# Optimization experiments

Measured on AMD Instinct MI355X. Metric: run time of the kernel, lower is better.

The kernel has to match this reference:

```python
import jax, jax.numpy as jnp
import numpy as np

B, S, D = 4, 2048, 512
H, DK = 8, 64
FFN = 2048
LEFT, CHUNK, RIGHT = 512, 128, 128
EPS = 1e-5


def _emformer_mask():
    # True = disallowed. Each query attends to its own chunk, LEFT keys before
    # the chunk start, and RIGHT keys after the chunk end.
    idx = jnp.arange(S)
    cs = (idx // CHUNK) * CHUNK                      # chunk start per query
    j = idx[None, :]
    allowed = (j >= cs[:, None] - LEFT) & (j < cs[:, None] + CHUNK + RIGHT)
    return jnp.broadcast_to(~allowed, (B, 1, S, S))


def _ln(x, g, b):
    m = jnp.mean(x, axis=-1, keepdims=True)
    v = jnp.var(x, axis=-1, keepdims=True)
    return (x - m) * jax.lax.rsqrt(v + EPS) * g + b


def setup_inputs() -> dict:
    key = jax.random.key(0)
    ks = jax.random.split(key, 8)
    w = lambda k, shp: jax.random.normal(k, shp, dtype=jnp.float32) * 0.02
    return {
        "x": jax.random.normal(ks[0], (B, S, D), dtype=jnp.float32),
        "mask": _emformer_mask(),
        "ln_in_g": jnp.ones((D,), jnp.float32), "ln_in_b": jnp.zeros((D,), jnp.float32),
        "wq": w(ks[1], (D, D)), "bq": jnp.zeros((D,), jnp.float32),
        "wk": w(ks[2], (D, D)), "bk": jnp.zeros((D,), jnp.float32),
        "wv": w(ks[3], (D, D)), "bv": jnp.zeros((D,), jnp.float32),
        "ln1_g": jnp.ones((D,), jnp.float32), "ln1_b": jnp.zeros((D,), jnp.float32),
        "w1": w(ks[4], (D, FFN)), "b1": jnp.zeros((FFN,), jnp.float32),
        "w2": w(ks[5], (FFN, D)), "b2": jnp.zeros((D,), jnp.float32),
        "ln2_g": jnp.ones((D,), jnp.float32), "ln2_b": jnp.zeros((D,), jnp.float32),
    }


def reference(x, mask, ln_in_g, ln_in_b, wq, bq, wk, bk, wv, bv,
              ln1_g, ln1_b, w1, b1, w2, b2, ln2_g, ln2_b):
    h = _ln(x, ln_in_g, ln_in_b)                                  # [B,S,D]
    q = (h @ wq + bq).reshape(B, S, H, DK).transpose(0, 2, 1, 3)   # [B,H,S,DK]
    k = (h @ wk + bk).reshape(B, S, H, DK).transpose(0, 2, 1, 3)
    v = (h @ wv + bv).reshape(B, S, H, DK).transpose(0, 2, 1, 3)
    scores = jnp.einsum("bhqd,bhkd->bhqk", q, k) / np.sqrt(DK).astype(np.float32)
    scores = jnp.where(mask, -jnp.inf, scores)
    probs = jax.nn.softmax(scores, axis=-1)
    probs = jnp.where(mask, 0.0, probs)                           # masked_fill after softmax
    out = jnp.einsum("bhqk,bhkd->bhqd", probs, v)
    out = out.transpose(0, 2, 1, 3).reshape(B, S, D)
    attn_out = out + h                                            # residual uses post-LN input
    o = _ln(attn_out, ln1_g, ln1_b)
    o = (o @ w1 + b1) @ w2 + b2 + attn_out                        # NOTE: no activation in source
    return _ln(o, ln2_g, ln2_b)
```

## Files before the change

### kernel.cpp

```cpp
#include <hip/hip_runtime.h>
#include <stdint.h>

#define B_ 4
#define S_ 2048
#define D_ 512
#define H_ 8
#define FFN_ 2048
#define M_ (B_*S_)

typedef unsigned short u16;
typedef __attribute__((ext_vector_type(8))) __bf16 bf16x8;
typedef __attribute__((ext_vector_type(8))) u16 u16x8;
typedef __attribute__((ext_vector_type(4))) float f32x4;

__device__ __forceinline__ u16 f2bf(float f) {
  uint32_t u = __builtin_bit_cast(uint32_t, f);
  u += 0x7FFFu + ((u >> 16) & 1u);
  return (u16)(u >> 16);
}
__device__ __forceinline__ bf16x8 ldfrag(const u16* p) {
  return __builtin_bit_cast(bf16x8, *(const u16x8*)p);
}
__device__ __forceinline__ void gld16(const void* g, void* l) {
  __builtin_amdgcn_global_load_lds(
      (const __attribute__((address_space(1))) void*)g,
      (__attribute__((address_space(3))) void*)l, 16, 0, 0);
}

__global__ __launch_bounds__(256)
void wtrans(const float* __restrict__ W, int K, int N, u16* __restrict__ Wt) {
  __shared__ float t[32][33];
  int n0 = blockIdx.x * 32, k0 = blockIdx.y * 32;
  int x = threadIdx.x, y = threadIdx.y;
#pragma unroll
  for (int r = 0; r < 4; r++) t[y + 8*r][x] = W[(size_t)(k0 + y + 8*r) * N + n0 + x];
  __syncthreads();
#pragma unroll
  for (int r = 0; r < 4; r++) Wt[(size_t)(n0 + y + 8*r) * K + k0 + x] = f2bf(t[x][y + 8*r]);
}

__global__ void bcat(const float* __restrict__ bq, const float* __restrict__ bk,
                     const float* __restrict__ bv, float* __restrict__ o) {
  int i = blockIdx.x * 256 + threadIdx.x;
  o[i] = i < 512 ? bq[i] : (i < 1024 ? bk[i - 512] : bv[i - 1024]);
}

template <bool OUT32, bool OUT16>
__global__ __launch_bounds__(128)
void ln_k(const float* __restrict__ x, const float* __restrict__ g,
          const float* __restrict__ bta, float* __restrict__ y32, u16* __restrict__ y16) {
  int row = blockIdx.x;
  int t = threadIdx.x;
  const float* xr = x + (size_t)row * 512;
  f32x4 v = *(const f32x4*)(xr + t * 4);
  float s = v.x + v.y + v.z + v.w;
  float s2 = v.x*v.x + v.y*v.y + v.z*v.z + v.w*v.w;
#pragma unroll
  for (int m = 32; m; m >>= 1) { s += __shfl_xor(s, m); s2 += __shfl_xor(s2, m); }
  __shared__ float p[4];
  int wv = t >> 6;
  if ((t & 63) == 0) { p[wv] = s; p[2 + wv] = s2; }
  __syncthreads();
  s = p[0] + p[1]; s2 = p[2] + p[3];
  float mean = s * (1.f / 512.f);
  float var = s2 * (1.f / 512.f) - mean * mean;
  float rs = rsqrtf(var + 1e-5f);
#pragma unroll
  for (int j = 0; j < 4; j++) {
    float o = (v[j] - mean) * rs * g[t*4 + j] + bta[t*4 + j];
    if constexpr (OUT32) y32[(size_t)row * 512 + t*4 + j] = o;
    if constexpr (OUT16) y16[(size_t)row * 512 + t*4 + j] = f2bf(o);
  }
}

template <bool RESID, bool OUT32, bool OUT16>
__global__ __launch_bounds__(256)
void gemm_bt(const u16* __restrict__ A, const u16* __restrict__ Bt,
             const float* __restrict__ bias, int K, int N,
             const float* __restrict__ resid, float* __restrict__ C32,
             u16* __restrict__ C16) {
  __shared__ __align__(16) u16 As[128 * 32];
  __shared__ __align__(16) u16 Bs[128 * 32];
  const int tid = threadIdx.x;
  const int wave = tid >> 6, lane = tid & 63;
  const int l15 = lane & 15, quad = lane >> 4;
  const int wm = wave >> 1, wn = wave & 1;
  const int row0 = blockIdx.y * 128, col0 = blockIdx.x * 128;

  f32x4 acc[4][4];
#pragma unroll
  for (int i = 0; i < 4; i++)
#pragma unroll
    for (int j = 0; j < 4; j++) acc[i][j] = (f32x4){0.f, 0.f, 0.f, 0.f};

  const int lr = lane >> 2, lc = (lane & 3) * 8;
  const int ch0 = wave * 2, ch1 = wave * 2 + 1;
  const u16* aG0 = A + (size_t)(row0 + ch0 * 16 + lr) * K + lc;
  const u16* aG1 = A + (size_t)(row0 + ch1 * 16 + lr) * K + lc;
  const u16* bG0 = Bt + (size_t)(col0 + ch0 * 16 + lr) * K + lc;
  const u16* bG1 = Bt + (size_t)(col0 + ch1 * 16 + lr) * K + lc;
  u16* aL0 = As + ch0 * 512 + lane * 8;
  u16* aL1 = As + ch1 * 512 + lane * 8;
  u16* bL0 = Bs + ch0 * 512 + lane * 8;
  u16* bL1 = Bs + ch1 * 512 + lane * 8;

  for (int k0 = 0; k0 < K; k0 += 32) {
    __syncthreads();
    gld16(aG0 + k0, aL0);
    gld16(aG1 + k0, aL1);
    gld16(bG0 + k0, bL0);
    gld16(bG1 + k0, bL1);
    __syncthreads();
    bf16x8 af[4], bf[4];
#pragma unroll
    for (int mt = 0; mt < 4; mt++) af[mt] = ldfrag(As + (wm*64 + mt*16 + l15) * 32 + quad * 8);
#pragma unroll
    for (int nt = 0; nt < 4; nt++) bf[nt] = ldfrag(Bs + (wn*64 + nt*16 + l15) * 32 + quad * 8);
#pragma unroll
    for (int mt = 0; mt < 4; mt++)
#pragma unroll
      for (int nt = 0; nt < 4; nt++)
        acc[mt][nt] = __builtin_amdgcn_mfma_f32_16x16x32_bf16(af[mt], bf[nt], acc[mt][nt], 0, 0, 0);
  }
#pragma unroll
  for (int mt = 0; mt < 4; mt++)
#pragma unroll
    for (int nt = 0; nt < 4; nt++) {
      int n = col0 + wn * 64 + nt * 16 + l15;
      float bv = bias[n];
#pragma unroll
      for (int r = 0; r < 4; r++) {
        int m = row0 + wm * 64 + mt * 16 + quad * 4 + r;
        float val = acc[mt][nt][r] + bv;
        if constexpr (RESID) val += resid[(size_t)m * N + n];
        if constexpr (OUT32) C32[(size_t)m * N + n] = val;
        if constexpr (OUT16) C16[(size_t)m * N + n] = f2bf(val);
      }
    }
}

__global__ __launch_bounds__(256)
void vtrans(const u16* __restrict__ qkv, u16* __restrict__ vt) {
  __shared__ u16 t[64][65];
  int s0 = blockIdx.x * 64, h = blockIdx.y, b = blockIdx.z;
  int x = threadIdx.x, y = threadIdx.y;
  const u16* src = qkv + (size_t)(b * 2048 + s0) * 1536 + 1024 + h * 64;
#pragma unroll
  for (int r = 0; r < 16; r++) { int s = y + 4*r; t[s][x] = src[(size_t)s * 1536 + x]; }
  __syncthreads();
  u16* dst = vt + (size_t)((b * 8 + h) * 64) * 2048 + s0;
#pragma unroll
  for (int r = 0; r < 16; r++) { int d = y + 4*r; dst[(size_t)d * 2048 + x] = t[x][d]; }
}

#define PSTR 136
__global__ __launch_bounds__(256)
void attn_k(const u16* __restrict__ qkv, const u16* __restrict__ vt,
            const float* __restrict__ hres, float* __restrict__ attn) {
  __shared__ __align__(16) u16 smem[8192 + 8192 + 64 * PSTR];
  u16* Ks = smem;
  u16* Vts = smem + 8192;
  u16* Ps = smem + 16384;
  u16* Qs = Ps;

  const int c2 = blockIdx.x, hh = blockIdx.y, b = blockIdx.z;
  const int c = c2 >> 1;
  const int s0 = c2 * 64;
  const int tid = threadIdx.x, wave = tid >> 6, lane = tid & 63;
  const int l15 = lane & 15, quad = lane >> 4;
  const int t_lo = (c > 4) ? c - 4 : 0;
  const int t_hi = (c + 2 < 16) ? c + 2 : 16;

  {
    int d8 = (lane & 7) * 8;
#pragma unroll
    for (int q2 = 0; q2 < 2; q2++) {
      int r = wave * 16 + q2 * 8 + (lane >> 3);
      gld16(qkv + (size_t)(b * 2048 + s0 + r) * 1536 + hh * 64 + d8, Qs + r * 64 + d8);
    }
  }
  __syncthreads();
  bf16x8 qf[2];
#pragma unroll
  for (int f = 0; f < 2; f++)
    qf[f] = ldfrag(Qs + (wave * 16 + l15) * 64 + f * 32 + quad * 8);

  f32x4 accO[4];
#pragma unroll
  for (int i = 0; i < 4; i++) accO[i] = (f32x4){0.f, 0.f, 0.f, 0.f};
  float den[4] = {0.f, 0.f, 0.f, 0.f};

  for (int kt = t_lo; kt < t_hi; ++kt) {
    __syncthreads();
    {
      int d8 = (lane & 7) * 8;
#pragma unroll
      for (int q2 = 0; q2 < 4; q2++) {
        int r = wave * 32 + q2 * 8 + (lane >> 3);
        gld16(qkv + (size_t)(b * 2048 + kt * 128 + r) * 1536 + 512 + hh * 64 + d8,
              Ks + r * 64 + d8);
      }
      int sp = (lane & 15) * 8;
#pragma unroll
      for (int q2 = 0; q2 < 4; q2++) {
        int d = (wave * 4 + q2) * 4 + (lane >> 4);
        gld16(vt + (size_t)((b * 8 + hh) * 64 + d) * 2048 + kt * 128 + sp,
              Vts + d * 128 + sp);
      }
    }
    __syncthreads();

    float pv[8][4];
#pragma unroll
    for (int nt = 0; nt < 8; nt++) {
      f32x4 s4 = (f32x4){0.f, 0.f, 0.f, 0.f};
#pragma unroll
      for (int f = 0; f < 2; f++) {
        bf16x8 kf = ldfrag(Ks + (nt * 16 + l15) * 64 + f * 32 + quad * 8);
        s4 = __builtin_amdgcn_mfma_f32_16x16x32_bf16(qf[f], kf, s4, 0, 0, 0);
      }
#pragma unroll
      for (int r = 0; r < 4; r++) {
        float pp = exp2f(s4[r] * (1.4426950408889634f * 0.125f));
        pv[nt][r] = pp;
        den[r] += pp;
      }
    }
#pragma unroll
    for (int nt = 0; nt < 8; nt++)
#pragma unroll
      for (int r = 0; r < 4; r++)
        Ps[(wave * 16 + quad * 4 + r) * PSTR + nt * 16 + l15] = f2bf(pv[nt][r]);
#pragma unroll
    for (int ki = 0; ki < 4; ki++) {
      bf16x8 pf = ldfrag(Ps + (wave * 16 + l15) * PSTR + ki * 32 + quad * 8);
#pragma unroll
      for (int dt = 0; dt < 4; dt++) {
        bf16x8 vf = ldfrag(Vts + (dt * 16 + l15) * 128 + ki * 32 + quad * 8);
        accO[dt] = __builtin_amdgcn_mfma_f32_16x16x32_bf16(pf, vf, accO[dt], 0, 0, 0);
      }
    }
  }
#pragma unroll
  for (int r = 0; r < 4; r++) {
    float d = den[r];
    d += __shfl_xor(d, 1); d += __shfl_xor(d, 2);
    d += __shfl_xor(d, 4); d += __shfl_xor(d, 8);
    den[r] = d;
  }
#pragma unroll
  for (int dt = 0; dt < 4; dt++)
#pragma unroll
    for (int r = 0; r < 4; r++) {
      int m = s0 + wave * 16 + quad * 4 + r;
      size_t idx = (size_t)(b * 2048 + m) * 512 + hh * 64 + dt * 16 + l15;
      attn[idx] = accO[dt][r] / den[r] + hres[idx];
    }
}

extern "C" void kernel_launch(void* const* d_in, const int* in_sizes, int n_in,
                              void* d_out, int out_size, void* d_ws, size_t ws_size,
                              hipStream_t stream) {
  (void)in_sizes; (void)n_in; (void)out_size; (void)ws_size;
  const float* x       = (const float*)d_in[0];
  const float* ln_in_g = (const float*)d_in[2];
  const float* ln_in_b = (const float*)d_in[3];
  const float* wq = (const float*)d_in[4];
  const float* bq = (const float*)d_in[5];
  const float* wk = (const float*)d_in[6];
  const float* bk = (const float*)d_in[7];
  const float* wv = (const float*)d_in[8];
  const float* bv = (const float*)d_in[9];
  const float* ln1_g = (const float*)d_in[10];
  const float* ln1_b = (const float*)d_in[11];
  const float* w1 = (const float*)d_in[12];
  const float* b1 = (const float*)d_in[13];
  const float* w2 = (const float*)d_in[14];
  const float* b2 = (const float*)d_in[15];
  const float* ln2_g = (const float*)d_in[16];
  const float* ln2_b = (const float*)d_in[17];

  char* ws = (char*)d_ws;
  size_t off = 0;
  auto alloc = [&](size_t bytes) {
    void* p = ws + off;
    off = (off + bytes + 255) & ~(size_t)255;
    return p;
  };
  u16*   wqkvt = (u16*)  alloc((size_t)1536 * 512 * 2);
  float* bqkv  = (float*)alloc(1536 * 4);
  u16*   w1t   = (u16*)  alloc((size_t)2048 * 512 * 2);
  u16*   w2t   = (u16*)  alloc((size_t)512 * 2048 * 2);
  float* h32   = (float*)alloc((size_t)M_ * 512 * 4);
  u16*   h16   = (u16*)  alloc((size_t)M_ * 512 * 2);
  u16*   qkv16 = (u16*)  alloc((size_t)M_ * 1536 * 2);
  u16*   vtb   = (u16*)  alloc((size_t)B_ * H_ * 64 * 2048 * 2);
  float* attn32= (float*)alloc((size_t)M_ * 512 * 4);
  float* out2  = h32;
  u16*   o16   = h16;
  u16*   f16b  = qkv16;

  wtrans<<<dim3(16, 16), dim3(32, 8), 0, stream>>>(wq, 512, 512, wqkvt);
  wtrans<<<dim3(16, 16), dim3(32, 8), 0, stream>>>(wk, 512, 512, wqkvt + (size_t)512 * 512);
  wtrans<<<dim3(16, 16), dim3(32, 8), 0, stream>>>(wv, 512, 512, wqkvt + (size_t)1024 * 512);
  wtrans<<<dim3(64, 16), dim3(32, 8), 0, stream>>>(w1, 512, 2048, w1t);
  wtrans<<<dim3(16, 64), dim3(32, 8), 0, stream>>>(w2, 2048, 512, w2t);
  bcat<<<6, 256, 0, stream>>>(bq, bk, bv, bqkv);

  ln_k<true, true><<<M_, 128, 0, stream>>>(x, ln_in_g, ln_in_b, h32, h16);
  gemm_bt<false, false, true><<<dim3(12, 64), 256, 0, stream>>>(
      h16, wqkvt, bqkv, 512, 1536, nullptr, nullptr, qkv16);
  vtrans<<<dim3(32, 8, 4), dim3(64, 4), 0, stream>>>(qkv16, vtb);
  attn_k<<<dim3(32, 8, 4), 256, 0, stream>>>(qkv16, vtb, h32, attn32);
  ln_k<false, true><<<M_, 128, 0, stream>>>(attn32, ln1_g, ln1_b, nullptr, o16);
  gemm_bt<false, false, true><<<dim3(16, 64), 256, 0, stream>>>(
      o16, w1t, b1, 512, 2048, nullptr, nullptr, f16b);
  gemm_bt<true, true, false><<<dim3(4, 64), 256, 0, stream>>>(
      f16b, w2t, b2, 2048, 512, attn32, out2, nullptr);
  ln_k<true, false><<<M_, 128, 0, stream>>>(out2, ln2_g, ln2_b, (float*)d_out, nullptr);
}
```

Baseline: 334.8 us.

## Swizzle LDS layouts, widen attention block to full chunk, narrow FFN2 tiles

```diff
diff --git a/kernel.cpp b/kernel.cpp
--- a/kernel.cpp
+++ b/kernel.cpp
@@ -73,60 +73,67 @@
   }
 }
 
-template <bool RESID, bool OUT32, bool OUT16>
+template <int NTW, bool RESID, bool OUT32, bool OUT16>
 __global__ __launch_bounds__(256)
 void gemm_bt(const u16* __restrict__ A, const u16* __restrict__ Bt,
              const float* __restrict__ bias, int K, int N,
              const float* __restrict__ resid, float* __restrict__ C32,
              u16* __restrict__ C16) {
   __shared__ __align__(16) u16 As[128 * 32];
-  __shared__ __align__(16) u16 Bs[128 * 32];
+  __shared__ __align__(16) u16 Bs[NTW * 1024];
   const int tid = threadIdx.x;
   const int wave = tid >> 6, lane = tid & 63;
   const int l15 = lane & 15, quad = lane >> 4;
   const int wm = wave >> 1, wn = wave & 1;
-  const int row0 = blockIdx.y * 128, col0 = blockIdx.x * 128;
-
-  f32x4 acc[4][4];
+  const int row0 = blockIdx.y * 128, col0 = blockIdx.x * (NTW * 32);
+
+  f32x4 acc[4][NTW];
 #pragma unroll
   for (int i = 0; i < 4; i++)
 #pragma unroll
-    for (int j = 0; j < 4; j++) acc[i][j] = (f32x4){0.f, 0.f, 0.f, 0.f};
-
-  const int lr = lane >> 2, lc = (lane & 3) * 8;
-  const int ch0 = wave * 2, ch1 = wave * 2 + 1;
-  const u16* aG0 = A + (size_t)(row0 + ch0 * 16 + lr) * K + lc;
-  const u16* aG1 = A + (size_t)(row0 + ch1 * 16 + lr) * K + lc;
-  const u16* bG0 = Bt + (size_t)(col0 + ch0 * 16 + lr) * K + lc;
-  const u16* bG1 = Bt + (size_t)(col0 + ch1 * 16 + lr) * K + lc;
-  u16* aL0 = As + ch0 * 512 + lane * 8;
-  u16* aL1 = As + ch1 * 512 + lane * 8;
-  u16* bL0 = Bs + ch0 * 512 + lane * 8;
-  u16* bL1 = Bs + ch1 * 512 + lane * 8;
+    for (int j = 0; j < NTW; j++) acc[i][j] = (f32x4){0.f, 0.f, 0.f, 0.f};
+
+  const int lr = lane >> 2;
+  const int lc = ((lane & 3) ^ ((lane >> 3) & 3)) * 8;
+  const u16* aG0 = A + (size_t)(row0 + (wave * 2) * 16 + lr) * K + lc;
+  const u16* aG1 = A + (size_t)(row0 + (wave * 2 + 1) * 16 + lr) * K + lc;
+  u16* aL0 = As + (wave * 2) * 512 + lane * 8;
+  u16* aL1 = As + (wave * 2 + 1) * 512 + lane * 8;
+  const u16* bG[NTW / 2];
+  u16* bL[NTW / 2];
+#pragma unroll
+  for (int i = 0; i < NTW / 2; i++) {
+    int ch = wave * (NTW / 2) + i;
+    bG[i] = Bt + (size_t)(col0 + ch * 16 + lr) * K + lc;
+    bL[i] = Bs + ch * 512 + lane * 8;
+  }
+  const int rsw = (l15 >> 1) & 3;
 
   for (int k0 = 0; k0 < K; k0 += 32) {
     __syncthreads();
     gld16(aG0 + k0, aL0);
     gld16(aG1 + k0, aL1);
-    gld16(bG0 + k0, bL0);
-    gld16(bG1 + k0, bL1);
+#pragma unroll
+    for (int i = 0; i < NTW / 2; i++) gld16(bG[i] + k0, bL[i]);
     __syncthreads();
-    bf16x8 af[4], bf[4];
-#pragma unroll
-    for (int mt = 0; mt < 4; mt++) af[mt] = ldfrag(As + (wm*64 + mt*16 + l15) * 32 + quad * 8);
-#pragma unroll
-    for (int nt = 0; nt < 4; nt++) bf[nt] = ldfrag(Bs + (wn*64 + nt*16 + l15) * 32 + quad * 8);
+    bf16x8 af[4], bf[NTW];
 #pragma unroll
     for (int mt = 0; mt < 4; mt++)
-#pragma unroll
-      for (int nt = 0; nt < 4; nt++)
+      af[mt] = ldfrag(As + (wm * 64 + mt * 16 + l15) * 32 + ((quad ^ rsw) * 8));
+#pragma unroll
+    for (int nt = 0; nt < NTW; nt++)
+      bf[nt] = ldfrag(Bs + (wn * (NTW * 16) + nt * 16 + l15) * 32 + ((quad ^ rsw) * 8));
+#pragma unroll
+    for (int mt = 0; mt < 4; mt++)
+#pragma unroll
+      for (int nt = 0; nt < NTW; nt++)
         acc[mt][nt] = __builtin_amdgcn_mfma_f32_16x16x32_bf16(af[mt], bf[nt], acc[mt][nt], 0, 0, 0);
   }
 #pragma unroll
   for (int mt = 0; mt < 4; mt++)
 #pragma unroll
-    for (int nt = 0; nt < 4; nt++) {
-      int n = col0 + wn * 64 + nt * 16 + l15;
+    for (int nt = 0; nt < NTW; nt++) {
+      int n = col0 + wn * (NTW * 16) + nt * 16 + l15;
       float bv = bias[n];
 #pragma unroll
       for (int r = 0; r < 4; r++) {
@@ -157,105 +164,118 @@
 __global__ __launch_bounds__(256)
 void attn_k(const u16* __restrict__ qkv, const u16* __restrict__ vt,
             const float* __restrict__ hres, float* __restrict__ attn) {
-  __shared__ __align__(16) u16 smem[8192 + 8192 + 64 * PSTR];
+  __shared__ __align__(16) u16 smem[8192 + 8192 + 128 * PSTR];
   u16* Ks = smem;
   u16* Vts = smem + 8192;
   u16* Ps = smem + 16384;
   u16* Qs = Ps;
 
-  const int c2 = blockIdx.x, hh = blockIdx.y, b = blockIdx.z;
-  const int c = c2 >> 1;
-  const int s0 = c2 * 64;
+  const int c = blockIdx.x, hh = blockIdx.y, b = blockIdx.z;
+  const int s0 = c * 128;
   const int tid = threadIdx.x, wave = tid >> 6, lane = tid & 63;
   const int l15 = lane & 15, quad = lane >> 4;
   const int t_lo = (c > 4) ? c - 4 : 0;
   const int t_hi = (c + 2 < 16) ? c + 2 : 16;
+  const int l7sw = l15 & 7;
 
   {
-    int d8 = (lane & 7) * 8;
-#pragma unroll
-    for (int q2 = 0; q2 < 2; q2++) {
-      int r = wave * 16 + q2 * 8 + (lane >> 3);
-      gld16(qkv + (size_t)(b * 2048 + s0 + r) * 1536 + hh * 64 + d8, Qs + r * 64 + d8);
+    const int cg = ((lane & 7) ^ (lane >> 3)) * 8;
+    const int cp = (lane & 7) * 8;
+#pragma unroll
+    for (int q2 = 0; q2 < 4; q2++) {
+      int r = wave * 32 + q2 * 8 + (lane >> 3);
+      gld16(qkv + (size_t)(b * 2048 + s0 + r) * 1536 + hh * 64 + cg, Qs + r * 64 + cp);
     }
   }
   __syncthreads();
-  bf16x8 qf[2];
-#pragma unroll
-  for (int f = 0; f < 2; f++)
-    qf[f] = ldfrag(Qs + (wave * 16 + l15) * 64 + f * 32 + quad * 8);
-
-  f32x4 accO[4];
-#pragma unroll
-  for (int i = 0; i < 4; i++) accO[i] = (f32x4){0.f, 0.f, 0.f, 0.f};
-  float den[4] = {0.f, 0.f, 0.f, 0.f};
+  bf16x8 qf[2][2];
+#pragma unroll
+  for (int qg = 0; qg < 2; qg++)
+#pragma unroll
+    for (int f = 0; f < 2; f++)
+      qf[qg][f] = ldfrag(Qs + (qg * 64 + wave * 16 + l15) * 64 + (((f * 4 + quad) ^ l7sw) * 8));
+
+  f32x4 accO[2][4];
+#pragma unroll
+  for (int qg = 0; qg < 2; qg++)
+#pragma unroll
+    for (int i = 0; i < 4; i++) accO[qg][i] = (f32x4){0.f, 0.f, 0.f, 0.f};
+  float den[2][4] = {{0.f, 0.f, 0.f, 0.f}, {0.f, 0.f, 0.f, 0.f}};
 
   for (int kt = t_lo; kt < t_hi; ++kt) {
     __syncthreads();
     {
-      int d8 = (lane & 7) * 8;
+      const int cgk = ((lane & 7) ^ (lane >> 3)) * 8;
+      const int cpk = (lane & 7) * 8;
 #pragma unroll
       for (int q2 = 0; q2 < 4; q2++) {
         int r = wave * 32 + q2 * 8 + (lane >> 3);
-        gld16(qkv + (size_t)(b * 2048 + kt * 128 + r) * 1536 + 512 + hh * 64 + d8,
-              Ks + r * 64 + d8);
-      }
-      int sp = (lane & 15) * 8;
+        gld16(qkv + (size_t)(b * 2048 + kt * 128 + r) * 1536 + 512 + hh * 64 + cgk,
+              Ks + r * 64 + cpk);
+      }
+      const int cpv = (lane & 15) * 8;
 #pragma unroll
       for (int q2 = 0; q2 < 4; q2++) {
         int d = (wave * 4 + q2) * 4 + (lane >> 4);
-        gld16(vt + (size_t)((b * 8 + hh) * 64 + d) * 2048 + kt * 128 + sp,
-              Vts + d * 128 + sp);
+        int cgv = ((lane & 8) | ((lane & 7) ^ (lane >> 4) ^ ((q2 & 1) << 2))) * 8;
+        gld16(vt + (size_t)((b * 8 + hh) * 64 + d) * 2048 + kt * 128 + cgv,
+              Vts + d * 128 + cpv);
       }
     }
     __syncthreads();
 
-    float pv[8][4];
 #pragma unroll
     for (int nt = 0; nt < 8; nt++) {
-      f32x4 s4 = (f32x4){0.f, 0.f, 0.f, 0.f};
-#pragma unroll
-      for (int f = 0; f < 2; f++) {
-        bf16x8 kf = ldfrag(Ks + (nt * 16 + l15) * 64 + f * 32 + quad * 8);
-        s4 = __builtin_amdgcn_mfma_f32_16x16x32_bf16(qf[f], kf, s4, 0, 0, 0);
-      }
+      bf16x8 kf0 = ldfrag(Ks + (nt * 16 + l15) * 64 + ((quad ^ l7sw) * 8));
+      bf16x8 kf1 = ldfrag(Ks + (nt * 16 + l15) * 64 + (((4 + quad) ^ l7sw) * 8));
+#pragma unroll
+      for (int qg = 0; qg < 2; qg++) {
+        f32x4 s4 = (f32x4){0.f, 0.f, 0.f, 0.f};
+        s4 = __builtin_amdgcn_mfma_f32_16x16x32_bf16(qf[qg][0], kf0, s4, 0, 0, 0);
+        s4 = __builtin_amdgcn_mfma_f32_16x16x32_bf16(qf[qg][1], kf1, s4, 0, 0, 0);
+#pragma unroll
+        for (int r = 0; r < 4; r++) {
+          float pp = exp2f(s4[r] * (1.4426950408889634f * 0.125f));
+          den[qg][r] += pp;
+          Ps[(qg * 64 + wave * 16 + quad * 4 + r) * PSTR + nt * 16 + l15] = f2bf(pp);
+        }
+      }
+    }
+#pragma unroll
+    for (int ki = 0; ki < 4; ki++) {
+      bf16x8 pf[2];
+#pragma unroll
+      for (int qg = 0; qg < 2; qg++)
+        pf[qg] = ldfrag(Ps + (qg * 64 + wave * 16 + l15) * PSTR + (ki * 4 + quad) * 8);
+#pragma unroll
+      for (int dt = 0; dt < 4; dt++) {
+        int g = ki * 4 + quad;
+        bf16x8 vf = ldfrag(Vts + (dt * 16 + l15) * 128 + (((g & 8) | ((g & 7) ^ l7sw)) * 8));
+#pragma unroll
+        for (int qg = 0; qg < 2; qg++)
+          accO[qg][dt] = __builtin_amdgcn_mfma_f32_16x16x32_bf16(pf[qg], vf, accO[qg][dt], 0, 0, 0);
+      }
+    }
+  }
+#pragma unroll
+  for (int qg = 0; qg < 2; qg++)
+#pragma unroll
+    for (int r = 0; r < 4; r++) {
+      float d = den[qg][r];
+      d += __shfl_xor(d, 1); d += __shfl_xor(d, 2);
+      d += __shfl_xor(d, 4); d += __shfl_xor(d, 8);
+      den[qg][r] = d;
+    }
+#pragma unroll
+  for (int qg = 0; qg < 2; qg++)
+#pragma unroll
+    for (int dt = 0; dt < 4; dt++)
 #pragma unroll
       for (int r = 0; r < 4; r++) {
-        float pp = exp2f(s4[r] * (1.4426950408889634f * 0.125f));
-        pv[nt][r] = pp;
-        den[r] += pp;
-      }
-    }
-#pragma unroll
-    for (int nt = 0; nt < 8; nt++)
-#pragma unroll
-      for (int r = 0; r < 4; r++)
-        Ps[(wave * 16 + quad * 4 + r) * PSTR + nt * 16 + l15] = f2bf(pv[nt][r]);
-#pragma unroll
-    for (int ki = 0; ki < 4; ki++) {
-      bf16x8 pf = ldfrag(Ps + (wave * 16 + l15) * PSTR + ki * 32 + quad * 8);
-#pragma unroll
-      for (int dt = 0; dt < 4; dt++) {
-        bf16x8 vf = ldfrag(Vts + (dt * 16 + l15) * 128 + ki * 32 + quad * 8);
-        accO[dt] = __builtin_amdgcn_mfma_f32_16x16x32_bf16(pf, vf, accO[dt], 0, 0, 0);
-      }
-    }
-  }
-#pragma unroll
-  for (int r = 0; r < 4; r++) {
-    float d = den[r];
-    d += __shfl_xor(d, 1); d += __shfl_xor(d, 2);
-    d += __shfl_xor(d, 4); d += __shfl_xor(d, 8);
-    den[r] = d;
-  }
-#pragma unroll
-  for (int dt = 0; dt < 4; dt++)
-#pragma unroll
-    for (int r = 0; r < 4; r++) {
-      int m = s0 + wave * 16 + quad * 4 + r;
-      size_t idx = (size_t)(b * 2048 + m) * 512 + hh * 64 + dt * 16 + l15;
-      attn[idx] = accO[dt][r] / den[r] + hres[idx];
-    }
+        int m = s0 + qg * 64 + wave * 16 + quad * 4 + r;
+        size_t idx = (size_t)(b * 2048 + m) * 512 + hh * 64 + dt * 16 + l15;
+        attn[idx] = accO[qg][dt][r] / den[qg][r] + hres[idx];
+      }
 }
 
 extern "C" void kernel_launch(void* const* d_in, const int* in_sizes, int n_in,
@@ -308,14 +328,14 @@
   bcat<<<6, 256, 0, stream>>>(bq, bk, bv, bqkv);
 
   ln_k<true, true><<<M_, 128, 0, stream>>>(x, ln_in_g, ln_in_b, h32, h16);
-  gemm_bt<false, false, true><<<dim3(12, 64), 256, 0, stream>>>(
+  gemm_bt<4, false, false, true><<<dim3(12, 64), 256, 0, stream>>>(
       h16, wqkvt, bqkv, 512, 1536, nullptr, nullptr, qkv16);
   vtrans<<<dim3(32, 8, 4), dim3(64, 4), 0, stream>>>(qkv16, vtb);
-  attn_k<<<dim3(32, 8, 4), 256, 0, stream>>>(qkv16, vtb, h32, attn32);
+  attn_k<<<dim3(16, 8, 4), 256, 0, stream>>>(qkv16, vtb, h32, attn32);
   ln_k<false, true><<<M_, 128, 0, stream>>>(attn32, ln1_g, ln1_b, nullptr, o16);
-  gemm_bt<false, false, true><<<dim3(16, 64), 256, 0, stream>>>(
+  gemm_bt<4, false, false, true><<<dim3(16, 64), 256, 0, stream>>>(
       o16, w1t, b1, 512, 2048, nullptr, nullptr, f16b);
-  gemm_bt<true, true, false><<<dim3(4, 64), 256, 0, stream>>>(
+  gemm_bt<2, true, true, false><<<dim3(8, 64), 256, 0, stream>>>(
       f16b, w2t, b2, 2048, 512, attn32, out2, nullptr);
   ln_k<true, false><<<M_, 128, 0, stream>>>(out2, ln2_g, ln2_b, (float*)d_out, nullptr);
 }
```

After: 308.1 us. 8.0% less time.
